# Performance work log

Measured on AMD Instinct MI355X. Metric: run time of the kernel, lower is better.

Reference implementation:

```python
import jax, jax.numpy as jnp
import numpy as np

B, T, C, H = 4, 2048, 512, 8
D = C // H  # dim_per_head = 64


def setup_inputs() -> dict:
    key = jax.random.key(0)
    ks = jax.random.split(key, 16)
    s = 1.0 / np.sqrt(C)
    return {
        "query": jax.random.normal(ks[0], (B, T, C), jnp.float32),
        "key": jax.random.normal(ks[1], (B, T, C), jnp.float32),
        "value": jax.random.normal(ks[2], (B, T, C), jnp.float32),
        "pos_embed": jax.random.normal(ks[3], (B, T, C), jnp.float32),
        "Wq": jax.random.normal(ks[4], (C, C), jnp.float32) * s,
        "bq": jnp.zeros((C,), jnp.float32),
        "Wk": jax.random.normal(ks[5], (C, C), jnp.float32) * s,
        "bk": jnp.zeros((C,), jnp.float32),
        "Wv": jax.random.normal(ks[6], (C, C), jnp.float32) * s,
        "bv": jnp.zeros((C,), jnp.float32),
        "Wpos": jax.random.normal(ks[7], (C, C), jnp.float32) * s,
        "pos_bias_u": jax.random.normal(ks[8], (H, D), jnp.float32) * 0.1,
        "pos_bias_v": jax.random.normal(ks[9], (H, D), jnp.float32) * 0.1,
        "Wo": jax.random.normal(ks[10], (C, C), jnp.float32) * s,
        "bo": jnp.zeros((C,), jnp.float32),
    }


def _relative_shift(pos_score):
    # pos_score: [B, H, T1, T2] -- Transformer-XL style shift
    b, h, t1, t2 = pos_score.shape
    padded = jnp.pad(pos_score, ((0, 0), (0, 0), (0, 0), (1, 0)))  # [B,H,T1,T2+1]
    padded = padded.reshape(b, h, t2 + 1, t1)
    return padded[:, :, 1:].reshape(b, h, t1, t2)


def reference(query, key, value, pos_embed, Wq, bq, Wk, bk, Wv, bv, Wpos,
              pos_bias_u, pos_bias_v, Wo, bo):
    q = (query @ Wq + bq).reshape(B, T, H, D)                    # b l h d
    k = (key @ Wk + bk).reshape(B, T, H, D)                      # b l h d
    v = (value @ Wv + bv).reshape(B, T, H, D)
    p = (pos_embed @ Wpos).reshape(B, T, H, D)
    # content score: (q + u) k^T ; pos score: (q + v) p^T
    content = jnp.einsum('bihd,bjhd->bhij', q + pos_bias_u, k)
    pos = jnp.einsum('bihd,bjhd->bhij', q + pos_bias_v, p)
    pos = _relative_shift(pos)
    scores = (content + pos) / jnp.sqrt(jnp.float32(D))
    attn = jax.nn.softmax(scores, axis=-1)
    ctx = jnp.einsum('bhij,bjhd->bihd', attn, v).reshape(B, T, C)
    return ctx @ Wo + bo
```

## Files before the change

### kernel.cpp

```cpp
#include <hip/hip_runtime.h>


#define Bb 4
#define Tt 2048
#define Cc 512
#define Hh 8
#define Dd 64

typedef __bf16 bf16_t;
typedef __bf16 bf16x8 __attribute__((ext_vector_type(8)));
typedef __bf16 bf16x4 __attribute__((ext_vector_type(4)));
typedef float  f32x4  __attribute__((ext_vector_type(4)));

__global__ __launch_bounds__(256, 4)
void wsplit_kernel(const float* __restrict__ Wq, const float* __restrict__ Wk,
                   const float* __restrict__ Wv, const float* __restrict__ Wp,
                   const float* __restrict__ Wo,
                   bf16_t* __restrict__ WT4, bf16_t* __restrict__ WoT, int mode)
{
    const int w = (mode < 0) ? (int)blockIdx.y : 4;
    const float* W = (w == 0) ? Wq : (w == 1) ? Wk : (w == 2) ? Wv : (w == 3) ? Wp : Wo;
    bf16_t* dh = (w == 4) ? WoT : WT4 + (size_t)w * 2 * 262144;
    bf16_t* dl = dh + 262144;

    const int tile = blockIdx.x;
    const int k0 = (tile >> 3) * 64;
    const int n0 = (tile & 7) * 64;
    const int tid = threadIdx.x;

    __shared__ bf16_t th[64][66];
    __shared__ bf16_t tl[64][66];

#pragma unroll
    for (int rep = 0; rep < 4; rep++) {
        int id = rep * 256 + tid;
        int kk = id >> 4, ns = id & 15;
        f32x4 v = *(const f32x4*)&W[(size_t)(k0 + kk) * 512 + n0 + ns * 4];
#pragma unroll
        for (int e = 0; e < 4; e++) {
            bf16_t h = (bf16_t)v[e];
            th[kk][ns * 4 + e] = h;
            tl[kk][ns * 4 + e] = (bf16_t)(v[e] - (float)h);
        }
    }
    __syncthreads();
#pragma unroll
    for (int rep = 0; rep < 2; rep++) {
        int id = rep * 256 + tid;
        int nn = id >> 3, ks = id & 7;
        bf16x8 hv, lv;
#pragma unroll
        for (int j = 0; j < 8; j++) { hv[j] = th[ks * 8 + j][nn]; lv[j] = tl[ks * 8 + j][nn]; }
        *(bf16x8*)&dh[(size_t)(n0 + nn) * 512 + k0 + ks * 8] = hv;
        *(bf16x8*)&dl[(size_t)(n0 + nn) * 512 + k0 + ks * 8] = lv;
    }
}

__global__ __launch_bounds__(256, 2)
void split_gemm_kernel(const float* __restrict__ Xq, const float* __restrict__ Xk,
                       const float* __restrict__ Xv, const float* __restrict__ Xp,
                       const float* __restrict__ Xc,
                       const bf16_t* __restrict__ WT4, const bf16_t* __restrict__ WoT,
                       const float* __restrict__ bq, const float* __restrict__ bk,
                       const float* __restrict__ bv, const float* __restrict__ bo,
                       const float* __restrict__ bias_u, const float* __restrict__ bias_v,
                       bf16_t* __restrict__ QU, bf16_t* __restrict__ QV,
                       bf16_t* __restrict__ K16, bf16_t* __restrict__ VT16,
                       bf16_t* __restrict__ P16, float* __restrict__ OUT,
                       int modeArg)
{
    const int z = (modeArg < 0) ? blockIdx.z : modeArg;
    const float* X    = (z == 0) ? Xq : (z == 1) ? Xk : (z == 2) ? Xv : (z == 3) ? Xp : Xc;
    const bf16_t* Wh  = (z == 4) ? WoT : WT4 + (size_t)z * 2 * 262144;
    const bf16_t* Wl  = Wh + 262144;
    const float* bias = (z == 0) ? bq : (z == 1) ? bk : (z == 2) ? bv : (z == 3) ? nullptr : bo;

    const int bx = blockIdx.x;
    const int g  = bx >> 3, x8 = bx & 7;
    const int mtile = (g >> 2) * 8 + x8;
    const int ntile = g & 3;
    const int r0 = mtile * 128;
    const int c0 = ntile * 128;

    const int tid  = threadIdx.x;
    const int wave = tid >> 6;
    const int lane = tid & 63;
    const int quad = lane >> 4;
    const int l16  = lane & 15;
    const int rb = (wave >> 1) * 64;
    const int cb = (wave & 1) * 64;

    __shared__ __align__(16) bf16_t Ah[128][72];
    __shared__ __align__(16) bf16_t Al[128][72];
    __shared__ __align__(16) bf16_t Bh[128][72];
    __shared__ __align__(16) bf16_t Bl[128][72];

    f32x4 acc[4][4];
#pragma unroll
    for (int mt = 0; mt < 4; mt++)
#pragma unroll
        for (int nt = 0; nt < 4; nt++)
#pragma unroll
            for (int r = 0; r < 4; r++) acc[mt][nt][r] = 0.f;

    f32x4  xa[8];
    bf16x8 wbh[4], wbl[4];

#pragma unroll
    for (int rep = 0; rep < 8; rep++) {
        int id = rep * 256 + tid;
        int m = id >> 4, c = id & 15;
        xa[rep] = *(const f32x4*)&X[(size_t)(r0 + m) * 512 + c * 4];
    }
#pragma unroll
    for (int rep = 0; rep < 4; rep++) {
        int id = rep * 256 + tid;
        int n = id >> 3, seg = id & 7;
        wbh[rep] = *(const bf16x8*)&Wh[(size_t)(c0 + n) * 512 + seg * 8];
        wbl[rep] = *(const bf16x8*)&Wl[(size_t)(c0 + n) * 512 + seg * 8];
    }

    for (int it = 0; it < 8; ++it) {
#pragma unroll
        for (int rep = 0; rep < 8; rep++) {
            int id = rep * 256 + tid;
            int m = id >> 4, c = id & 15;
            f32x4 v = xa[rep];
            bf16x4 hh, ll;
#pragma unroll
            for (int e = 0; e < 4; e++) {
                bf16_t hv = (bf16_t)v[e];
                hh[e] = hv;
                ll[e] = (bf16_t)(v[e] - (float)hv);
            }
            *(bf16x4*)&Ah[m][c * 4] = hh;
            *(bf16x4*)&Al[m][c * 4] = ll;
        }
#pragma unroll
        for (int rep = 0; rep < 4; rep++) {
            int id = rep * 256 + tid;
            int n = id >> 3, seg = id & 7;
            *(bf16x8*)&Bh[n][seg * 8] = wbh[rep];
            *(bf16x8*)&Bl[n][seg * 8] = wbl[rep];
        }
        __syncthreads();

        if (it < 7) {
            const int k0n = (it + 1) * 64;
#pragma unroll
            for (int rep = 0; rep < 8; rep++) {
                int id = rep * 256 + tid;
                int m = id >> 4, c = id & 15;
                xa[rep] = *(const f32x4*)&X[(size_t)(r0 + m) * 512 + k0n + c * 4];
            }
#pragma unroll
            for (int rep = 0; rep < 4; rep++) {
                int id = rep * 256 + tid;
                int n = id >> 3, seg = id & 7;
                wbh[rep] = *(const bf16x8*)&Wh[(size_t)(c0 + n) * 512 + k0n + seg * 8];
                wbl[rep] = *(const bf16x8*)&Wl[(size_t)(c0 + n) * 512 + k0n + seg * 8];
            }
        }

#pragma unroll
        for (int kc = 0; kc < 2; kc++) {
            bf16x8 bh[4], bl[4], ah[4], al[4];
#pragma unroll
            for (int nt = 0; nt < 4; nt++) {
                bh[nt] = *(const bf16x8*)&Bh[cb + nt * 16 + l16][kc * 32 + quad * 8];
                bl[nt] = *(const bf16x8*)&Bl[cb + nt * 16 + l16][kc * 32 + quad * 8];
            }
#pragma unroll
            for (int mt = 0; mt < 4; mt++) {
                ah[mt] = *(const bf16x8*)&Ah[rb + mt * 16 + l16][kc * 32 + quad * 8];
                al[mt] = *(const bf16x8*)&Al[rb + mt * 16 + l16][kc * 32 + quad * 8];
            }
#pragma unroll
            for (int mt = 0; mt < 4; mt++) {
#pragma unroll
                for (int nt = 0; nt < 4; nt++) {
                    acc[mt][nt] = __builtin_amdgcn_mfma_f32_16x16x32_bf16(ah[mt], bh[nt], acc[mt][nt], 0, 0, 0);
                    acc[mt][nt] = __builtin_amdgcn_mfma_f32_16x16x32_bf16(ah[mt], bl[nt], acc[mt][nt], 0, 0, 0);
                    acc[mt][nt] = __builtin_amdgcn_mfma_f32_16x16x32_bf16(al[mt], bh[nt], acc[mt][nt], 0, 0, 0);
                }
            }
        }
        __syncthreads();
    }

#pragma unroll
    for (int mt = 0; mt < 4; mt++) {
#pragma unroll
        for (int r = 0; r < 4; r++) {
            int row = r0 + rb + mt * 16 + quad * 4 + r;
#pragma unroll
            for (int nt = 0; nt < 4; nt++) {
                int col = c0 + cb + nt * 16 + l16;
                float y = acc[mt][nt][r] + (bias ? bias[col] : 0.f);
                if (z == 4) {
                    OUT[(size_t)row * 512 + col] = y;
                } else {
                    int b = row >> 11, t = row & 2047;
                    int h = col >> 6,  d = col & 63;
                    if (z == 0) {
                        size_t idx = (((size_t)(b * Hh + h)) * Tt + t) * Dd + d;
                        QU[idx] = (bf16_t)(y + bias_u[col]);
                        QV[idx] = (bf16_t)(y + bias_v[col]);
                    } else if (z == 1) {
                        size_t idx = (((size_t)(b * Hh + h)) * Tt + t) * Dd + d;
                        K16[idx] = (bf16_t)y;
                    } else if (z == 2) {
                        size_t idx = (((size_t)(b * Hh + h)) * Dd + d) * Tt + t;
                        VT16[idx] = (bf16_t)y;
                    } else {
                        size_t idx = (((size_t)(b * Hh + h)) * Tt + t) * Dd + d;
                        P16[idx] = (bf16_t)y;
                    }
                }
            }
        }
    }
}

__global__ __launch_bounds__(256, 3)
void attn_kernel(const bf16_t* __restrict__ QU, const bf16_t* __restrict__ QV,
                 const bf16_t* __restrict__ K16, const bf16_t* __restrict__ VT16,
                 const bf16_t* __restrict__ P16, float* __restrict__ CTX)
{
    const int bh = blockIdx.x;
    const int i0 = blockIdx.y * 64;
    const int b = bh >> 3, h = bh & 7;
    const int tid = threadIdx.x;
    const int wave = tid >> 6;
    const int lane = tid & 63;
    const int quad = lane >> 4;
    const int l16 = lane & 15;

    const bf16_t* qu_g = QU + (size_t)bh * Tt * Dd;
    const bf16_t* qv_g = QV + (size_t)bh * Tt * Dd;
    const bf16_t* k_g  = K16 + (size_t)bh * Tt * Dd;
    const bf16_t* vt_g = VT16 + (size_t)bh * Dd * Tt;
    const bf16_t* p_g  = P16 + (size_t)bh * Tt * Dd;

    __shared__ __align__(16) char smem[38912];
    bf16_t (*pA)[72]  = (bf16_t (*)[72])(smem);
    bf16_t (*k_s)[72] = (bf16_t (*)[72])(smem + 18432);
    bf16_t (*msw)[88] = (bf16_t (*)[88])(smem + 27648);

    const int off_w = 48 - wave * 16;
    const int cmin = 48 - wave * 16;
    const int cmax = 126 - wave * 16;

    const int qrow = i0 + wave * 16 + l16;
    const int qrow2 = (qrow + 1 > Tt - 1) ? (Tt - 1) : (qrow + 1);
    bf16x8 aq[2], av1[2], av2[2];
#pragma unroll
    for (int kc = 0; kc < 2; kc++) {
        aq[kc]  = *(const bf16x8*)(qu_g + (size_t)qrow  * Dd + kc * 32 + quad * 8);
        av1[kc] = *(const bf16x8*)(qv_g + (size_t)qrow  * Dd + kc * 32 + quad * 8);
        av2[kc] = *(const bf16x8*)(qv_g + (size_t)qrow2 * Dd + kc * 32 + quad * 8);
    }

    float lsum[4];
    f32x4 accO[4];
#pragma unroll
    for (int r = 0; r < 4; r++) lsum[r] = 0.f;
#pragma unroll
    for (int dt = 0; dt < 4; dt++)
#pragma unroll
        for (int r = 0; r < 4; r++) accO[dt][r] = 0.f;

    for (int j0 = 0; j0 < Tt; j0 += 64) {
        int d_lo = i0 - (j0 + 63);
        int d_hi = i0 + 63 - j0;
        int w1 = 0, prow1 = 0;
        if (d_hi >= 0) {
            int b1 = d_lo > 0 ? d_lo : 0;
            w1 = d_hi - b1 + 1;
            prow1 = (Tt - 1) - d_hi;
        }
        int dmax2 = d_hi < -2 ? d_hi : -2;
        int w2 = 0, e_lo = 0;
        if (d_lo <= dmax2) {
            e_lo = -dmax2 - 2;
            int e_hi = -d_lo - 2;
            w2 = e_hi - e_lo + 1;
        }
        int c2_0 = d_hi + 2 + e_lo;
        int nct1 = (w1 + 15) >> 4;
        int nct2 = (w2 + 15) >> 4;

        for (int idx = tid; idx < 64 * 8; idx += 256) {
            int row = idx >> 3, seg = idx & 7;
            *(f32x4*)&k_s[row][seg * 8] = *(const f32x4*)(k_g + (size_t)(j0 + row) * Dd + seg * 8);
        }
        for (int idx = tid; idx < (w1 + w2) * 8; idx += 256) {
            int rr = idx >> 3, seg = idx & 7;
            int srcrow = (rr < w1) ? (prow1 + rr) : (e_lo + rr - w1);
            *(f32x4*)&pA[rr][seg * 8] = *(const f32x4*)(p_g + (size_t)srcrow * Dd + seg * 8);
        }
        __syncthreads();

        f32x4 accS[4];
#pragma unroll
        for (int nt = 0; nt < 4; nt++) {
            f32x4 acc = {0.f, 0.f, 0.f, 0.f};
#pragma unroll
            for (int kc = 0; kc < 2; kc++) {
                bf16x8 bk8 = *(const bf16x8*)&k_s[nt * 16 + l16][kc * 32 + quad * 8];
                acc = __builtin_amdgcn_mfma_f32_16x16x32_bf16(aq[kc], bk8, acc, 0, 0, 0);
            }
            accS[nt] = acc;
        }

        for (int ct = 0; ct < nct1 + nct2; ct++) {
            bool b2 = ct >= nct1;
            int rb_ = b2 ? (w1 + (ct - nct1) * 16) : (ct * 16);
            int cb_ = b2 ? (c2_0 + (ct - nct1) * 16) : (ct * 16);
            if (cb_ > cmax || cb_ + 15 < cmin) continue;
            f32x4 acc = {0.f, 0.f, 0.f, 0.f};
#pragma unroll
            for (int kc = 0; kc < 2; kc++) {
                bf16x8 bp = *(const bf16x8*)&pA[rb_ + l16][kc * 32 + quad * 8];
                acc = b2 ? __builtin_amdgcn_mfma_f32_16x16x32_bf16(av2[kc], bp, acc, 0, 0, 0)
                         : __builtin_amdgcn_mfma_f32_16x16x32_bf16(av1[kc], bp, acc, 0, 0, 0);
            }
            int colp = cb_ + l16 - off_w;
            if ((unsigned)colp < 80u) {
#pragma unroll
                for (int r = 0; r < 4; r++)
                    msw[wave * 16 + quad * 4 + r][colp] = (bf16_t)acc[r];
            }
        }
        {
            int zcl = d_hi + 1 - off_w;
            if ((unsigned)zcl < 80u && quad == 0)
                msw[wave * 16 + l16][zcl] = (bf16_t)0.f;
        }

        float wv[4][4];
#pragma unroll
        for (int nt = 0; nt < 4; nt++) {
#pragma unroll
            for (int r = 0; r < 4; r++) {
                float pos = (float)msw[wave * 16 + quad * 4 + r]
                                    [nt * 16 + l16 + 15 - (quad * 4 + r)];
                float x = accS[nt][r] + pos;
                float a = fminf(fmaf(x, 0.18033688f, -17.3123405f), 120.0f);
                float w = exp2f(a);
                lsum[r] += w;
                wv[nt][r] = w;
            }
        }
#pragma unroll
        for (int nt = 0; nt < 4; nt++)
#pragma unroll
            for (int r = 0; r < 4; r++)
                msw[wave * 16 + quad * 4 + r][nt * 16 + l16] = (bf16_t)wv[nt][r];

#pragma unroll
        for (int kc = 0; kc < 2; kc++) {
            bf16x8 aw = *(const bf16x8*)&msw[wave * 16 + l16][kc * 32 + quad * 8];
#pragma unroll
            for (int dt = 0; dt < 4; dt++) {
                bf16x8 bv8 = *(const bf16x8*)(vt_g + (size_t)(dt * 16 + l16) * Tt + j0 + kc * 32 + quad * 8);
                accO[dt] = __builtin_amdgcn_mfma_f32_16x16x32_bf16(aw, bv8, accO[dt], 0, 0, 0);
            }
        }
        __syncthreads();
    }

#pragma unroll
    for (int r = 0; r < 4; r++) {
#pragma unroll
        for (int off = 1; off < 16; off <<= 1) lsum[r] += __shfl_xor(lsum[r], off, 64);
    }

#pragma unroll
    for (int r = 0; r < 4; r++) {
        int il = wave * 16 + quad * 4 + r;
        int ig = i0 + il;
        float inv = 1.0f / lsum[r];
#pragma unroll
        for (int dt = 0; dt < 4; dt++) {
            CTX[((size_t)(b * Tt + ig)) * Cc + h * Dd + dt * 16 + l16] = accO[dt][r] * inv;
        }
    }
}

extern "C" void kernel_launch(void* const* d_in, const int* in_sizes, int n_in,
                              void* d_out, int out_size, void* d_ws, size_t ws_size,
                              hipStream_t stream)
{
    const float* query = (const float*)d_in[0];
    const float* key   = (const float*)d_in[1];
    const float* value = (const float*)d_in[2];
    const float* pemb  = (const float*)d_in[3];
    const float* Wq    = (const float*)d_in[4];
    const float* bq    = (const float*)d_in[5];
    const float* Wk    = (const float*)d_in[6];
    const float* bk    = (const float*)d_in[7];
    const float* Wv    = (const float*)d_in[8];
    const float* bv    = (const float*)d_in[9];
    const float* Wpos  = (const float*)d_in[10];
    const float* pbu   = (const float*)d_in[11];
    const float* pbv   = (const float*)d_in[12];
    const float* Wo    = (const float*)d_in[13];
    const float* bo    = (const float*)d_in[14];

    const size_t NE = (size_t)Bb * Hh * Tt * Dd;
    bf16_t* QU   = (bf16_t*)d_ws;
    bf16_t* QV   = QU + NE;
    bf16_t* K16  = QV + NE;
    bf16_t* VT16 = K16 + NE;
    bf16_t* P16  = VT16 + NE;
    float*  CTX  = (float*)(P16 + NE);

    bf16_t* WT4 = (bf16_t*)CTX;
    bf16_t* WoT = (bf16_t*)QU;

    wsplit_kernel<<<dim3(64, 4), 256, 0, stream>>>(Wq, Wk, Wv, Wpos, Wo, WT4, WoT, -1);

    split_gemm_kernel<<<dim3(256, 1, 4), 256, 0, stream>>>(
        query, key, value, pemb, CTX, WT4, WoT,
        bq, bk, bv, bo, pbu, pbv, QU, QV, K16, VT16, P16, (float*)d_out, -1);

    attn_kernel<<<dim3(32, 32), 256, 0, stream>>>(QU, QV, K16, VT16, P16, CTX);

    wsplit_kernel<<<dim3(64, 1), 256, 0, stream>>>(Wq, Wk, Wv, Wpos, Wo, WT4, WoT, 4);

    split_gemm_kernel<<<dim3(256, 1, 1), 256, 0, stream>>>(
        query, key, value, pemb, CTX, WT4, WoT,
        bq, bk, bv, bo, pbu, pbv, QU, QV, K16, VT16, P16, (float*)d_out, 4);
}
```

Before: 441.2 us.

## Split projection GEMM with shallower K-tile and add dedicated smaller-tile output GEMM

The QKVP projection GEMM now uses a 32-wide K step (16 iterations) with smaller shared-memory tiles and fewer staging registers, and its launch bound rises to 3 blocks per SM. The aim is higher occupancy to hide global-load and conversion latency. The output projection moves to its own kernel with 64-row tiles and 512 blocks, so the 8192x512 GEMM fills more CUs instead of 256 large blocks. In exchange there are more barriers per block and less reuse per tile.

Result: no change. 432.7 us (-1.9%).

```diff
diff --git a/kernel.cpp b/kernel.cpp
--- a/kernel.cpp
+++ b/kernel.cpp
@@ -56,24 +56,22 @@
     }
 }
 
-__global__ __launch_bounds__(256, 2)
+__global__ __launch_bounds__(256, 3)
 void split_gemm_kernel(const float* __restrict__ Xq, const float* __restrict__ Xk,
                        const float* __restrict__ Xv, const float* __restrict__ Xp,
-                       const float* __restrict__ Xc,
-                       const bf16_t* __restrict__ WT4, const bf16_t* __restrict__ WoT,
+                       const bf16_t* __restrict__ WT4,
                        const float* __restrict__ bq, const float* __restrict__ bk,
-                       const float* __restrict__ bv, const float* __restrict__ bo,
+                       const float* __restrict__ bv,
                        const float* __restrict__ bias_u, const float* __restrict__ bias_v,
                        bf16_t* __restrict__ QU, bf16_t* __restrict__ QV,
                        bf16_t* __restrict__ K16, bf16_t* __restrict__ VT16,
-                       bf16_t* __restrict__ P16, float* __restrict__ OUT,
-                       int modeArg)
+                       bf16_t* __restrict__ P16)
 {
-    const int z = (modeArg < 0) ? blockIdx.z : modeArg;
-    const float* X    = (z == 0) ? Xq : (z == 1) ? Xk : (z == 2) ? Xv : (z == 3) ? Xp : Xc;
-    const bf16_t* Wh  = (z == 4) ? WoT : WT4 + (size_t)z * 2 * 262144;
+    const int z = blockIdx.z;
+    const float* X    = (z == 0) ? Xq : (z == 1) ? Xk : (z == 2) ? Xv : Xp;
+    const bf16_t* Wh  = WT4 + (size_t)z * 2 * 262144;
     const bf16_t* Wl  = Wh + 262144;
-    const float* bias = (z == 0) ? bq : (z == 1) ? bk : (z == 2) ? bv : (z == 3) ? nullptr : bo;
+    const float* bias = (z == 0) ? bq : (z == 1) ? bk : (z == 2) ? bv : nullptr;
 
     const int bx = blockIdx.x;
     const int g  = bx >> 3, x8 = bx & 7;
@@ -90,27 +88,173 @@
     const int rb = (wave >> 1) * 64;
     const int cb = (wave & 1) * 64;
 
-    __shared__ __align__(16) bf16_t Ah[128][72];
-    __shared__ __align__(16) bf16_t Al[128][72];
+    __shared__ __align__(16) bf16_t Ah[128][40];
+    __shared__ __align__(16) bf16_t Al[128][40];
+    __shared__ __align__(16) bf16_t Bh[128][40];
+    __shared__ __align__(16) bf16_t Bl[128][40];
+
+    f32x4 acc[4][4];
+#pragma unroll
+    for (int mt = 0; mt < 4; mt++)
+#pragma unroll
+        for (int nt = 0; nt < 4; nt++)
+#pragma unroll
+            for (int r = 0; r < 4; r++) acc[mt][nt][r] = 0.f;
+
+    f32x4  xa[4];
+    bf16x8 wbh[2], wbl[2];
+
+#pragma unroll
+    for (int rep = 0; rep < 4; rep++) {
+        int id = rep * 256 + tid;
+        int m = id >> 3, c = id & 7;
+        xa[rep] = *(const f32x4*)&X[(size_t)(r0 + m) * 512 + c * 4];
+    }
+#pragma unroll
+    for (int rep = 0; rep < 2; rep++) {
+        int id = rep * 256 + tid;
+        int n = id >> 2, seg = id & 3;
+        wbh[rep] = *(const bf16x8*)&Wh[(size_t)(c0 + n) * 512 + seg * 8];
+        wbl[rep] = *(const bf16x8*)&Wl[(size_t)(c0 + n) * 512 + seg * 8];
+    }
+
+    for (int it = 0; it < 16; ++it) {
+#pragma unroll
+        for (int rep = 0; rep < 4; rep++) {
+            int id = rep * 256 + tid;
+            int m = id >> 3, c = id & 7;
+            f32x4 v = xa[rep];
+            bf16x4 hh, ll;
+#pragma unroll
+            for (int e = 0; e < 4; e++) {
+                bf16_t hv = (bf16_t)v[e];
+                hh[e] = hv;
+                ll[e] = (bf16_t)(v[e] - (float)hv);
+            }
+            *(bf16x4*)&Ah[m][c * 4] = hh;
+            *(bf16x4*)&Al[m][c * 4] = ll;
+        }
+#pragma unroll
+        for (int rep = 0; rep < 2; rep++) {
+            int id = rep * 256 + tid;
+            int n = id >> 2, seg = id & 3;
+            *(bf16x8*)&Bh[n][seg * 8] = wbh[rep];
+            *(bf16x8*)&Bl[n][seg * 8] = wbl[rep];
+        }
+        __syncthreads();
+
+        if (it < 15) {
+            const int k0n = (it + 1) * 32;
+#pragma unroll
+            for (int rep = 0; rep < 4; rep++) {
+                int id = rep * 256 + tid;
+                int m = id >> 3, c = id & 7;
+                xa[rep] = *(const f32x4*)&X[(size_t)(r0 + m) * 512 + k0n + c * 4];
+            }
+#pragma unroll
+            for (int rep = 0; rep < 2; rep++) {
+                int id = rep * 256 + tid;
+                int n = id >> 2, seg = id & 3;
+                wbh[rep] = *(const bf16x8*)&Wh[(size_t)(c0 + n) * 512 + k0n + seg * 8];
+                wbl[rep] = *(const bf16x8*)&Wl[(size_t)(c0 + n) * 512 + k0n + seg * 8];
+            }
+        }
+
+        {
+            bf16x8 bh[4], bl[4], ah[4], al[4];
+#pragma unroll
+            for (int nt = 0; nt < 4; nt++) {
+                bh[nt] = *(const bf16x8*)&Bh[cb + nt * 16 + l16][quad * 8];
+                bl[nt] = *(const bf16x8*)&Bl[cb + nt * 16 + l16][quad * 8];
+            }
+#pragma unroll
+            for (int mt = 0; mt < 4; mt++) {
+                ah[mt] = *(const bf16x8*)&Ah[rb + mt * 16 + l16][quad * 8];
+                al[mt] = *(const bf16x8*)&Al[rb + mt * 16 + l16][quad * 8];
+            }
+#pragma unroll
+            for (int mt = 0; mt < 4; mt++) {
+#pragma unroll
+                for (int nt = 0; nt < 4; nt++) {
+                    acc[mt][nt] = __builtin_amdgcn_mfma_f32_16x16x32_bf16(ah[mt], bh[nt], acc[mt][nt], 0, 0, 0);
+                    acc[mt][nt] = __builtin_amdgcn_mfma_f32_16x16x32_bf16(ah[mt], bl[nt], acc[mt][nt], 0, 0, 0);
+                    acc[mt][nt] = __builtin_amdgcn_mfma_f32_16x16x32_bf16(al[mt], bh[nt], acc[mt][nt], 0, 0, 0);
+                }
+            }
+        }
+        __syncthreads();
+    }
+
+#pragma unroll
+    for (int mt = 0; mt < 4; mt++) {
+#pragma unroll
+        for (int r = 0; r < 4; r++) {
+            int row = r0 + rb + mt * 16 + quad * 4 + r;
+#pragma unroll
+            for (int nt = 0; nt < 4; nt++) {
+                int col = c0 + cb + nt * 16 + l16;
+                float y = acc[mt][nt][r] + (bias ? bias[col] : 0.f);
+                int b = row >> 11, t = row & 2047;
+                int h = col >> 6,  d = col & 63;
+                if (z == 0) {
+                    size_t idx = (((size_t)(b * Hh + h)) * Tt + t) * Dd + d;
+                    QU[idx] = (bf16_t)(y + bias_u[col]);
+                    QV[idx] = (bf16_t)(y + bias_v[col]);
+                } else if (z == 1) {
+                    size_t idx = (((size_t)(b * Hh + h)) * Tt + t) * Dd + d;
+                    K16[idx] = (bf16_t)y;
+                } else if (z == 2) {
+                    size_t idx = (((size_t)(b * Hh + h)) * Dd + d) * Tt + t;
+                    VT16[idx] = (bf16_t)y;
+                } else {
+                    size_t idx = (((size_t)(b * Hh + h)) * Tt + t) * Dd + d;
+                    P16[idx] = (bf16_t)y;
+                }
+            }
+        }
+    }
+}
+
+__global__ __launch_bounds__(256, 2)
+void out_gemm_kernel(const float* __restrict__ Xc, const bf16_t* __restrict__ WoT,
+                     const float* __restrict__ bo, float* __restrict__ OUT)
+{
+    const bf16_t* Wh = WoT;
+    const bf16_t* Wl = WoT + 262144;
+
+    const int bx = blockIdx.x;
+    const int r0 = (bx >> 2) * 64;
+    const int c0 = (bx & 3) * 128;
+
+    const int tid  = threadIdx.x;
+    const int wave = tid >> 6;
+    const int lane = tid & 63;
+    const int quad = lane >> 4;
+    const int l16  = lane & 15;
+    const int rb = (wave >> 1) * 32;
+    const int cb = (wave & 1) * 64;
+
+    __shared__ __align__(16) bf16_t Ah[64][72];
+    __shared__ __align__(16) bf16_t Al[64][72];
     __shared__ __align__(16) bf16_t Bh[128][72];
     __shared__ __align__(16) bf16_t Bl[128][72];
 
-    f32x4 acc[4][4];
-#pragma unroll
-    for (int mt = 0; mt < 4; mt++)
+    f32x4 acc[2][4];
+#pragma unroll
+    for (int mt = 0; mt < 2; mt++)
 #pragma unroll
         for (int nt = 0; nt < 4; nt++)
 #pragma unroll
             for (int r = 0; r < 4; r++) acc[mt][nt][r] = 0.f;
 
-    f32x4  xa[8];
+    f32x4  xa[4];
     bf16x8 wbh[4], wbl[4];
 
 #pragma unroll
-    for (int rep = 0; rep < 8; rep++) {
+    for (int rep = 0; rep < 4; rep++) {
         int id = rep * 256 + tid;
         int m = id >> 4, c = id & 15;
-        xa[rep] = *(const f32x4*)&X[(size_t)(r0 + m) * 512 + c * 4];
+        xa[rep] = *(const f32x4*)&Xc[(size_t)(r0 + m) * 512 + c * 4];
     }
 #pragma unroll
     for (int rep = 0; rep < 4; rep++) {
@@ -122,7 +266,7 @@
 
     for (int it = 0; it < 8; ++it) {
 #pragma unroll
-        for (int rep = 0; rep < 8; rep++) {
+        for (int rep = 0; rep < 4; rep++) {
             int id = rep * 256 + tid;
             int m = id >> 4, c = id & 15;
             f32x4 v = xa[rep];
@@ -148,10 +292,10 @@
         if (it < 7) {
             const int k0n = (it + 1) * 64;
 #pragma unroll
-            for (int rep = 0; rep < 8; rep++) {
+            for (int rep = 0; rep < 4; rep++) {
                 int id = rep * 256 + tid;
                 int m = id >> 4, c = id & 15;
-                xa[rep] = *(const f32x4*)&X[(size_t)(r0 + m) * 512 + k0n + c * 4];
+                xa[rep] = *(const f32x4*)&Xc[(size_t)(r0 + m) * 512 + k0n + c * 4];
             }
 #pragma unroll
             for (int rep = 0; rep < 4; rep++) {
@@ -164,19 +308,19 @@
 
 #pragma unroll
         for (int kc = 0; kc < 2; kc++) {
-            bf16x8 bh[4], bl[4], ah[4], al[4];
+            bf16x8 bh[4], bl[4], ah[2], al[2];
 #pragma unroll
             for (int nt = 0; nt < 4; nt++) {
                 bh[nt] = *(const bf16x8*)&Bh[cb + nt * 16 + l16][kc * 32 + quad * 8];
                 bl[nt] = *(const bf16x8*)&Bl[cb + nt * 16 + l16][kc * 32 + quad * 8];
             }
 #pragma unroll
-            for (int mt = 0; mt < 4; mt++) {
+            for (int mt = 0; mt < 2; mt++) {
                 ah[mt] = *(const bf16x8*)&Ah[rb + mt * 16 + l16][kc * 32 + quad * 8];
                 al[mt] = *(const bf16x8*)&Al[rb + mt * 16 + l16][kc * 32 + quad * 8];
             }
 #pragma unroll
-            for (int mt = 0; mt < 4; mt++) {
+            for (int mt = 0; mt < 2; mt++) {
 #pragma unroll
                 for (int nt = 0; nt < 4; nt++) {
                     acc[mt][nt] = __builtin_amdgcn_mfma_f32_16x16x32_bf16(ah[mt], bh[nt], acc[mt][nt], 0, 0, 0);
@@ -189,34 +333,14 @@
     }
 
 #pragma unroll
-    for (int mt = 0; mt < 4; mt++) {
+    for (int mt = 0; mt < 2; mt++) {
 #pragma unroll
         for (int r = 0; r < 4; r++) {
             int row = r0 + rb + mt * 16 + quad * 4 + r;
 #pragma unroll
             for (int nt = 0; nt < 4; nt++) {
                 int col = c0 + cb + nt * 16 + l16;
-                float y = acc[mt][nt][r] + (bias ? bias[col] : 0.f);
-                if (z == 4) {
-                    OUT[(size_t)row * 512 + col] = y;
-                } else {
-                    int b = row >> 11, t = row & 2047;
-                    int h = col >> 6,  d = col & 63;
-                    if (z == 0) {
-                        size_t idx = (((size_t)(b * Hh + h)) * Tt + t) * Dd + d;
-                        QU[idx] = (bf16_t)(y + bias_u[col]);
-                        QV[idx] = (bf16_t)(y + bias_v[col]);
-                    } else if (z == 1) {
-                        size_t idx = (((size_t)(b * Hh + h)) * Tt + t) * Dd + d;
-                        K16[idx] = (bf16_t)y;
-                    } else if (z == 2) {
-                        size_t idx = (((size_t)(b * Hh + h)) * Dd + d) * Tt + t;
-                        VT16[idx] = (bf16_t)y;
-                    } else {
-                        size_t idx = (((size_t)(b * Hh + h)) * Tt + t) * Dd + d;
-                        P16[idx] = (bf16_t)y;
-                    }
-                }
+                OUT[(size_t)row * 512 + col] = acc[mt][nt][r] + bo[col];
             }
         }
     }
@@ -422,14 +546,12 @@
     wsplit_kernel<<<dim3(64, 4), 256, 0, stream>>>(Wq, Wk, Wv, Wpos, Wo, WT4, WoT, -1);
 
     split_gemm_kernel<<<dim3(256, 1, 4), 256, 0, stream>>>(
-        query, key, value, pemb, CTX, WT4, WoT,
-        bq, bk, bv, bo, pbu, pbv, QU, QV, K16, VT16, P16, (float*)d_out, -1);
+        query, key, value, pemb, WT4,
+        bq, bk, bv, pbu, pbv, QU, QV, K16, VT16, P16);
 
     attn_kernel<<<dim3(32, 32), 256, 0, stream>>>(QU, QV, K16, VT16, P16, CTX);
 
     wsplit_kernel<<<dim3(64, 1), 256, 0, stream>>>(Wq, Wk, Wv, Wpos, Wo, WT4, WoT, 4);
 
-    split_gemm_kernel<<<dim3(256, 1, 1), 256, 0, stream>>>(
-        query, key, value, pemb, CTX, WT4, WoT,
-        bq, bk, bv, bo, pbu, pbv, QU, QV, K16, VT16, P16, (float*)d_out, 4);
+    out_gemm_kernel<<<dim3(512), 256, 0, stream>>>(CTX, WoT, bo, (float*)d_out);
 }
```
